# Kernel tuning notes

Measured on AMD Instinct MI355X. Metric: run time of the kernel, lower is better.

The kernel has to match this reference:

```python
import jax, jax.numpy as jnp
import numpy as np

C = 112       # channels, divisible by NCHUNK
NCHUNK = 7    # shift_sizes[0]
PAD = 3       # shift_sizes[0] // 2
EPS = 1e-5


def _gn(x, g, b):
    # GroupNorm(1, C): normalize over (C, D, H, W) per sample, per-channel affine
    mu = jnp.mean(x, axis=(1, 2, 3, 4), keepdims=True)
    var = jnp.mean((x - mu) ** 2, axis=(1, 2, 3, 4), keepdims=True)
    xn = (x - mu) * jax.lax.rsqrt(var + EPS)
    return xn * g[None, :, None, None, None] + b[None, :, None, None, None]


def _conv1x1(x, w, b):
    # 1x1x1 Conv3d == channel-mixing GEMM
    return jnp.einsum('oc,bcdhw->bodhw', w, x) + b[None, :, None, None, None]


def _gelu(x):
    return jax.nn.gelu(x, approximate=False)  # torch nn.GELU default = exact erf


def _pad3(x):
    return jnp.pad(x, ((0, 0), (0, 0), (PAD, PAD), (PAD, PAD), (PAD, PAD)))


def _axial_shift(xp, axis, D, H, W):
    # chunk channels into NCHUNK groups, roll group i by (i - PAD) along `axis`,
    # concat, then narrow each spatial axis at offset PAD with ORIGINAL lengths
    chunks = jnp.split(xp, NCHUNK, axis=1)
    shifted = [jnp.roll(c, s, axis=axis) for c, s in zip(chunks, range(-PAD, PAD + 1))]
    xc = jnp.concatenate(shifted, axis=1)
    return xc[:, :, PAD:PAD + D, PAD:PAD + H, PAD:PAD + W]


def setup_inputs() -> dict:
    key = jax.random.key(0)
    ks = jax.random.split(key, 9)
    B, D, H, W = 1, 64, 64, 64
    hid = 4 * C

    def w(k, shape, fan_in):
        return jax.random.normal(k, shape, jnp.float32) * np.float32(1.0 / np.sqrt(fan_in))

    return {
        'x': jax.random.normal(ks[0], (B, C, D, H, W), jnp.float32),
        'conv1_w': w(ks[1], (C, C), C), 'conv1_b': jnp.zeros((C,), jnp.float32),
        'conv2d_w': w(ks[2], (C, C), C), 'conv2d_b': jnp.zeros((C,), jnp.float32),
        'conv2h_w': w(ks[3], (C, C), C), 'conv2h_b': jnp.zeros((C,), jnp.float32),
        'conv2w_w': w(ks[4], (C, C), C), 'conv2w_b': jnp.zeros((C,), jnp.float32),
        'conv3_w': w(ks[5], (C, C), C), 'conv3_b': jnp.zeros((C,), jnp.float32),
        'fc1_w': w(ks[6], (hid, C), C), 'fc1_b': jnp.zeros((hid,), jnp.float32),
        'fc2_w': w(ks[7], (C, hid), hid), 'fc2_b': jnp.zeros((C,), jnp.float32),
        'n1_g': jnp.ones((C,), jnp.float32), 'n1_b': jnp.zeros((C,), jnp.float32),
        'na1_g': jnp.ones((C,), jnp.float32), 'na1_b': jnp.zeros((C,), jnp.float32),
        'na2_g': jnp.ones((C,), jnp.float32), 'na2_b': jnp.zeros((C,), jnp.float32),
        'n2_g': jnp.ones((C,), jnp.float32), 'n2_b': jnp.zeros((C,), jnp.float32),
    }


def reference(x, conv1_w, conv1_b, conv2d_w, conv2d_b, conv2h_w, conv2h_b,
              conv2w_w, conv2w_b, conv3_w, conv3_b, fc1_w, fc1_b, fc2_w, fc2_b,
              n1_g, n1_b, na1_g, na1_b, na2_g, na2_b, n2_g, n2_b):
    B, _, D, H, W = x.shape
    shortcut = x
    h0 = _gn(x, n1_g, n1_b)                                   # block norm1

    # ---- AxialShift.axial_shift_single_scale ----
    a = _gelu(_gn(_conv1x1(h0, conv1_w, conv1_b), na1_g, na1_b))
    xp = _pad3(a)                                             # padded once (D branch)
    x_d = _gelu(_conv1x1(_axial_shift(xp, 2, D, H, W), conv2d_w, conv2d_b))
    xp = _pad3(xp)                                            # padded twice (H branch, as in source)
    x_h = _gelu(_conv1x1(_axial_shift(xp, 3, D, H, W), conv2h_w, conv2h_b))
    xp = _pad3(xp)                                            # padded thrice (W branch)
    x_w = _gelu(_conv1x1(_axial_shift(xp, 4, D, H, W), conv2w_w, conv2w_b))
    y = _conv1x1(_gn(x_d + x_h + x_w, na2_g, na2_b), conv3_w, conv3_b)
    y = y + h0                                                # AxialShift residual (x_masked == 0)

    x1 = shortcut + y                                         # block residual 1
    m = _gn(x1, n2_g, n2_b)                                   # block norm2
    m = _conv1x1(_gelu(_conv1x1(m, fc1_w, fc1_b)), fc2_w, fc2_b)  # Mlp (drop=0)
    return x1 + m
```

## Files before the change

### kernel.cpp

```cpp
#include <hip/hip_runtime.h>
#include <math.h>

static constexpr int CH   = 112;
static constexpr int HID  = 448;
static constexpr int NPOS = 64 * 64 * 64;
static constexpr long long NELEM = (long long)CH * NPOS;

typedef _Float16 f16x8 __attribute__((ext_vector_type(8)));
typedef _Float16 f16x4 __attribute__((ext_vector_type(4)));
typedef float    f32x4 __attribute__((ext_vector_type(4)));

__device__ __forceinline__ float gelu_f(float x) {
    float ax = fabsf(x) * 0.70710678118654752f;
    float t  = __builtin_amdgcn_rcpf(1.0f + 0.3275911f * ax);
    float p  = t * (0.254829592f + t * (-0.284496736f + t * (1.421413741f +
               t * (-1.453152027f + t * 1.061405429f))));
    float e  = exp2f(-1.4426950408889634f * ax * ax);
    float er = 1.0f - p * e;
    er = (x < 0.f) ? -er : er;
    return 0.5f * x * (1.0f + er);
}

__device__ __forceinline__ void stats_from(const double* __restrict__ S, float* mu, float* inv) {
    double m = S[0] / (double)NELEM;
    double v = S[1] / (double)NELEM - m * m;
    *mu  = (float)m;
    *inv = (float)(1.0 / sqrt(v + 1e-5));
}

__device__ __forceinline__ void block_reduce2(double s, double q, double* __restrict__ out) {
    #pragma unroll
    for (int off = 32; off > 0; off >>= 1) {
        s += __shfl_down(s, off, 64);
        q += __shfl_down(q, off, 64);
    }
    __shared__ double red[16];
    int lane = threadIdx.x & 63, wv = threadIdx.x >> 6;
    int nw = blockDim.x >> 6;
    if (lane == 0) { red[wv] = s; red[wv + 8] = q; }
    __syncthreads();
    if (threadIdx.x == 0) {
        double S = 0, Q = 0;
        for (int i = 0; i < nw; i++) { S += red[i]; Q += red[i + 8]; }
        atomicAdd(out, S);
        atomicAdd(out + 1, Q);
    }
}

__device__ __forceinline__ void mfma_tile(const _Float16* __restrict__ w,
                                          const _Float16 (*lsT)[136],
                                          int l15, int l4, int wv, f32x4 acc[7]) {
    #pragma unroll
    for (int kk = 0; kk < 4; kk++) {
        f16x8 b = *(const f16x8*)(&lsT[wv * 16 + l15][kk * 32 + l4 * 8]);
        #pragma unroll
        for (int mt = 0; mt < 7; mt++) {
            f16x8 a = *(const f16x8*)(w + (mt * 16 + l15) * 128 + kk * 32 + l4 * 8);
            acc[mt] = __builtin_amdgcn_mfma_f32_16x16x32_f16(a, b, acc[mt], 0, 0, 0);
        }
    }
}

__device__ __forceinline__ void accum_gelu(f32x4 tot[7], const f32x4 acc[7],
                                           const float* __restrict__ b, int l4) {
    #pragma unroll
    for (int mt = 0; mt < 7; mt++) {
        float4 bb = *(const float4*)(b + mt * 16 + l4 * 4);
        tot[mt][0] += gelu_f(acc[mt][0] + bb.x);
        tot[mt][1] += gelu_f(acc[mt][1] + bb.y);
        tot[mt][2] += gelu_f(acc[mt][2] + bb.z);
        tot[mt][3] += gelu_f(acc[mt][3] + bb.w);
    }
}

__global__ void k_reduce(const float* __restrict__ x, double* __restrict__ S) {
    long long i0 = (long long)blockIdx.x * blockDim.x + threadIdx.x;
    long long stride = (long long)gridDim.x * blockDim.x;
    const float4* x4 = (const float4*)x;
    long long n4 = NELEM / 4;
    double s = 0, q = 0;
    for (long long i = i0; i < n4; i += stride) {
        float4 v = x4[i];
        s += (double)v.x + (double)v.y + (double)v.z + (double)v.w;
        q += (double)v.x * v.x + (double)v.y * v.y + (double)v.z * v.z + (double)v.w * v.w;
    }
    block_reduce2(s, q, S);
}

__global__ void k_fold(const double* __restrict__ S, const float* __restrict__ w,
                       const float* __restrict__ b, const float* __restrict__ g,
                       const float* __restrict__ bta,
                       _Float16* __restrict__ w16, float* __restrict__ beff) {
    int o = blockIdx.x;
    float mu, inv; stats_from(S, &mu, &inv);
    float partial = 0.f;
    for (int c = threadIdx.x; c < 128; c += blockDim.x) {
        float wv_ = 0.f, contrib = 0.f;
        if (c < CH) {
            float sc = inv * g[c];
            float sh = bta[c] - mu * sc;
            float w0 = w[o * CH + c];
            wv_ = w0 * sc;
            contrib = w0 * sh;
        }
        w16[o * 128 + c] = (_Float16)wv_;
        partial += contrib;
    }
    #pragma unroll
    for (int off = 32; off > 0; off >>= 1) partial += __shfl_down(partial, off, 64);
    __shared__ float rp[2];
    int lane = threadIdx.x & 63, wv_ = threadIdx.x >> 6;
    if (lane == 0) rp[wv_] = partial;
    __syncthreads();
    if (threadIdx.x == 0) beff[o] = b[o] + rp[0] + rp[1];
}

__global__ void k_cast(const float* __restrict__ w2d, const float* __restrict__ w2h,
                       const float* __restrict__ w2w, const float* __restrict__ fc2w,
                       _Float16* __restrict__ w2dh, _Float16* __restrict__ w2hh,
                       _Float16* __restrict__ w2wh, _Float16* __restrict__ fc2h) {
    int b = blockIdx.x;
    if (b < CH) {
        for (int c = threadIdx.x; c < 128; c += blockDim.x) {
            float vd = 0.f, vh = 0.f, vw = 0.f;
            if (c < CH) { vd = w2d[b * CH + c]; vh = w2h[b * CH + c]; vw = w2w[b * CH + c]; }
            w2dh[b * 128 + c] = (_Float16)vd;
            w2hh[b * 128 + c] = (_Float16)vh;
            w2wh[b * 128 + c] = (_Float16)vw;
        }
    }
    for (int i = threadIdx.x; i < CH; i += blockDim.x)
        fc2h[b * CH + i] = (_Float16)fc2w[b * CH + i];
}

__global__ void __launch_bounds__(256, 2)
k_conv1(const float* __restrict__ x, const _Float16* __restrict__ w1h,
        const float* __restrict__ b1e, _Float16* __restrict__ t16, double* __restrict__ S1) {
    __shared__ __align__(16) _Float16 lxT[64][136];
    int tid = threadIdx.x, lane = tid & 63, wv = tid >> 6, l15 = lane & 15, l4 = lane >> 4;
    int pos0 = blockIdx.x * 64;

    {
        int c0 = tid >> 4, q = tid & 15;
        #pragma unroll
        for (int p = 0; p < 7; p++) {
            int c = p * 16 + c0;
            float4 v = *(const float4*)(x + (long long)c * NPOS + pos0 + q * 4);
            lxT[q * 4 + 0][c] = (_Float16)v.x;
            lxT[q * 4 + 1][c] = (_Float16)v.y;
            lxT[q * 4 + 2][c] = (_Float16)v.z;
            lxT[q * 4 + 3][c] = (_Float16)v.w;
        }
        for (int i = tid; i < 64 * 16; i += 256) lxT[i >> 4][112 + (i & 15)] = (_Float16)0.f;
    }
    __syncthreads();

    f32x4 acc[7];
    {
        f32x4 z = {0.f, 0.f, 0.f, 0.f};
        #pragma unroll
        for (int mt = 0; mt < 7; mt++) acc[mt] = z;
    }
    mfma_tile(w1h, lxT, l15, l4, wv, acc);

    long long posw = pos0 + wv * 16 + l15;
    double s = 0, q = 0;
    #pragma unroll
    for (int mt = 0; mt < 7; mt++) {
        int ob = mt * 16 + l4 * 4;
        float4 bb = *(const float4*)(b1e + ob);
        const float* bp = (const float*)&bb;
        f16x4 o4;
        #pragma unroll
        for (int r = 0; r < 4; r++) {
            float tv = acc[mt][r] + bp[r];
            o4[r] = (_Float16)tv;
            s += (double)tv; q += (double)tv * tv;
        }
        *(f16x4*)(t16 + posw * 128 + ob) = o4;
    }
    {
        f16x4 z4; z4[0] = z4[1] = z4[2] = z4[3] = (_Float16)0.f;
        *(f16x4*)(t16 + posw * 128 + 112 + l4 * 4) = z4;
    }
    block_reduce2(s, q, S1);
}

__global__ void k_act(const _Float16* __restrict__ t16, _Float16* __restrict__ a16,
                      const double* __restrict__ S1, const float* __restrict__ g,
                      const float* __restrict__ bta) {
    float mu, inv; stats_from(S1, &mu, &inv);
    long long i8 = (long long)blockIdx.x * blockDim.x + threadIdx.x;
    int c = (int)((i8 * 8) & 127);
    f16x8 r;
    if (c < 112) {
        f16x8 v = *(const f16x8*)(t16 + i8 * 8);
        float4 g0 = *(const float4*)(g + c);
        float4 g1 = *(const float4*)(g + c + 4);
        float4 b0 = *(const float4*)(bta + c);
        float4 b1 = *(const float4*)(bta + c + 4);
        const float* gp0 = (const float*)&g0; const float* gp1 = (const float*)&g1;
        const float* bp0 = (const float*)&b0; const float* bp1 = (const float*)&b1;
        #pragma unroll
        for (int j = 0; j < 4; j++) {
            float sc = inv * gp0[j], sh = bp0[j] - mu * sc;
            r[j] = (_Float16)gelu_f((float)v[j] * sc + sh);
        }
        #pragma unroll
        for (int j = 0; j < 4; j++) {
            float sc = inv * gp1[j], sh = bp1[j] - mu * sc;
            r[4 + j] = (_Float16)gelu_f((float)v[4 + j] * sc + sh);
        }
    } else {
        #pragma unroll
        for (int j = 0; j < 8; j++) r[j] = (_Float16)0.f;
    }
    *(f16x8*)(a16 + i8 * 8) = r;
}

__global__ void __launch_bounds__(256, 2)
k_shift(const _Float16* __restrict__ a16,
        const _Float16* __restrict__ w2dh, const float* __restrict__ b2d,
        const _Float16* __restrict__ w2hh, const float* __restrict__ b2h,
        const _Float16* __restrict__ w2wh, const float* __restrict__ b2w,
        _Float16* __restrict__ s16, double* __restrict__ S2) {
    __shared__ __align__(16) _Float16 lsT[64][136];
    int tid = threadIdx.x, lane = tid & 63, wv = tid >> 6, l15 = lane & 15, l4 = lane >> 4;
    int d = blockIdx.x >> 6, h = blockIdx.x & 63;

    f32x4 tot[7], acc[7];
    {
        f32x4 z = {0.f, 0.f, 0.f, 0.f};
        #pragma unroll
        for (int mt = 0; mt < 7; mt++) tot[mt] = z;
    }
    f16x8 z8;
    #pragma unroll
    for (int j = 0; j < 8; j++) z8[j] = (_Float16)0.f;

    for (int u = tid; u < 1024; u += 256) {
        int w = u >> 4, u16 = u & 15;
        f16x8 v = z8;
        if (u16 < 14) {
            int p = u16 >> 1;
            int dd = d - (p - 3);
            if ((unsigned)dd < 64u)
                v = *(const f16x8*)(a16 + (long long)(dd * 4096 + h * 64 + w) * 128 + u16 * 8);
        }
        *(f16x8*)(&lsT[w][u16 * 8]) = v;
    }
    __syncthreads();
    {
        f32x4 z = {0.f, 0.f, 0.f, 0.f};
        #pragma unroll
        for (int mt = 0; mt < 7; mt++) acc[mt] = z;
    }
    mfma_tile(w2dh, lsT, l15, l4, wv, acc);
    accum_gelu(tot, acc, b2d, l4);
    __syncthreads();

    {
        int dd = d - 3;
        bool dok = (unsigned)dd < 64u;
        for (int u = tid; u < 1024; u += 256) {
            int w = u >> 4, u16 = u & 15;
            f16x8 v = z8;
            if (u16 < 14) {
                int p = u16 >> 1;
                int hh = h - p;
                int ww = w - 3;
                if (dok && (unsigned)hh < 64u && ww >= 0)
                    v = *(const f16x8*)(a16 + (long long)(dd * 4096 + hh * 64 + ww) * 128 + u16 * 8);
            }
            *(f16x8*)(&lsT[w][u16 * 8]) = v;
        }
    }
    __syncthreads();
    {
        f32x4 z = {0.f, 0.f, 0.f, 0.f};
        #pragma unroll
        for (int mt = 0; mt < 7; mt++) acc[mt] = z;
    }
    mfma_tile(w2hh, lsT, l15, l4, wv, acc);
    accum_gelu(tot, acc, b2h, l4);
    __syncthreads();

    {
        int dd = d - 6, hh = h - 6;
        bool ok = ((unsigned)dd < 64u) && ((unsigned)hh < 64u);
        for (int u = tid; u < 1024; u += 256) {
            int w = u >> 4, u16 = u & 15;
            f16x8 v = z8;
            if (ok && u16 < 14) {
                int p = u16 >> 1;
                int ww = w - 3 - p;
                if ((unsigned)ww < 64u)
                    v = *(const f16x8*)(a16 + (long long)(dd * 4096 + hh * 64 + ww) * 128 + u16 * 8);
            }
            *(f16x8*)(&lsT[w][u16 * 8]) = v;
        }
    }
    __syncthreads();
    {
        f32x4 z = {0.f, 0.f, 0.f, 0.f};
        #pragma unroll
        for (int mt = 0; mt < 7; mt++) acc[mt] = z;
    }
    mfma_tile(w2wh, lsT, l15, l4, wv, acc);
    accum_gelu(tot, acc, b2w, l4);

    long long posw = d * 4096 + h * 64 + wv * 16 + l15;
    double s = 0, q = 0;
    #pragma unroll
    for (int mt = 0; mt < 7; mt++) {
        f16x4 o4;
        #pragma unroll
        for (int r = 0; r < 4; r++) {
            float sv = tot[mt][r];
            o4[r] = (_Float16)sv;
            s += (double)sv; q += (double)sv * sv;
        }
        *(f16x4*)(s16 + posw * 128 + mt * 16 + l4 * 4) = o4;
    }
    {
        f16x4 z4; z4[0] = z4[1] = z4[2] = z4[3] = (_Float16)0.f;
        *(f16x4*)(s16 + posw * 128 + 112 + l4 * 4) = z4;
    }
    block_reduce2(s, q, S2);
}

__global__ void __launch_bounds__(256, 2)
k_comb(const _Float16* s16, const float* __restrict__ x,
       const _Float16* __restrict__ w3h, const float* __restrict__ b3e,
       const double* __restrict__ S0, const float* __restrict__ n1g,
       const float* __restrict__ n1b, float* __restrict__ x1,
       _Float16* x1h, double* __restrict__ S3) {
    __shared__ __align__(16) _Float16 lsT[64][136];
    int tid = threadIdx.x, lane = tid & 63, wv = tid >> 6, l15 = lane & 15, l4 = lane >> 4;
    int pos0 = blockIdx.x * 64;

    for (int u = tid; u < 1024; u += 256) {
        int w = u >> 4, u16 = u & 15;
        *(f16x8*)(&lsT[w][u16 * 8]) =
            *(const f16x8*)(s16 + (long long)(pos0 + w) * 128 + u16 * 8);
    }
    __syncthreads();

    f32x4 acc[7];
    {
        f32x4 z = {0.f, 0.f, 0.f, 0.f};
        #pragma unroll
        for (int mt = 0; mt < 7; mt++) acc[mt] = z;
    }
    mfma_tile(w3h, lsT, l15, l4, wv, acc);

    float mu, inv; stats_from(S0, &mu, &inv);
    long long posw = pos0 + wv * 16 + l15;
    double s = 0, q = 0;
    #pragma unroll
    for (int mt = 0; mt < 7; mt++) {
        int ob = mt * 16 + l4 * 4;
        float4 b3 = *(const float4*)(b3e + ob);
        float4 g4 = *(const float4*)(n1g + ob);
        float4 n4 = *(const float4*)(n1b + ob);
        const float* b3p = (const float*)&b3;
        const float* g4p = (const float*)&g4;
        const float* n4p = (const float*)&n4;
        f16x4 o4;
        #pragma unroll
        for (int r = 0; r < 4; r++) {
            int o = ob + r;
            float y  = acc[mt][r] + b3p[r];
            float xv = x[(long long)o * NPOS + posw];
            float sc = inv * g4p[r];
            float h0 = xv * sc + (n4p[r] - mu * sc);
            float v  = xv + y + h0;
            x1[(long long)o * NPOS + posw] = v;
            o4[r] = (_Float16)v;
            s += (double)v; q += (double)v * v;
        }
        *(f16x4*)(x1h + posw * 128 + ob) = o4;
    }
    block_reduce2(s, q, S3);
}

__global__ void __launch_bounds__(256, 3)
k_mlp(float* __restrict__ x1out, const _Float16* __restrict__ x1h,
      const _Float16* __restrict__ fc1h, const float* __restrict__ b1m,
      const _Float16* __restrict__ fc2h, const float* __restrict__ fc2b) {
    __shared__ __align__(16) char smem[64 * 232 * 2];
    _Float16 (*lxT)[136] = (_Float16 (*)[136])smem;
    _Float16 (*GT)[232]  = (_Float16 (*)[232])smem;
    int tid = threadIdx.x, lane = tid & 63, wv = tid >> 6, l15 = lane & 15, l4 = lane >> 4;
    int pos0 = blockIdx.x * 64;

    for (int u = tid; u < 1024; u += 256) {
        int w = u >> 4, u16 = u & 15;
        *(f16x8*)(&lxT[w][u16 * 8]) =
            *(const f16x8*)(x1h + (long long)(pos0 + w) * 128 + u16 * 8);
    }
    __syncthreads();

    int hb = wv * 112;
    f32x4 acc1[7][4];
    {
        f32x4 z = {0.f, 0.f, 0.f, 0.f};
        #pragma unroll
        for (int mt = 0; mt < 7; mt++)
            #pragma unroll
            for (int nt = 0; nt < 4; nt++) acc1[mt][nt] = z;
    }
    #pragma unroll
    for (int kk = 0; kk < 4; kk++) {
        f16x8 a[7];
        #pragma unroll
        for (int mt = 0; mt < 7; mt++)
            a[mt] = *(const f16x8*)(fc1h + (hb + mt * 16 + l15) * 128 + kk * 32 + l4 * 8);
        #pragma unroll
        for (int nt = 0; nt < 4; nt++) {
            f16x8 b = *(const f16x8*)(&lxT[nt * 16 + l15][kk * 32 + l4 * 8]);
            #pragma unroll
            for (int mt = 0; mt < 7; mt++)
                acc1[mt][nt] = __builtin_amdgcn_mfma_f32_16x16x32_f16(a[mt], b, acc1[mt][nt], 0, 0, 0);
        }
    }
    f16x4 g16[7][4];
    #pragma unroll
    for (int mt = 0; mt < 7; mt++) {
        float4 bias = *(const float4*)(b1m + hb + mt * 16 + l4 * 4);
        #pragma unroll
        for (int nt = 0; nt < 4; nt++) {
            g16[mt][nt][0] = (_Float16)gelu_f(acc1[mt][nt][0] + bias.x);
            g16[mt][nt][1] = (_Float16)gelu_f(acc1[mt][nt][1] + bias.y);
            g16[mt][nt][2] = (_Float16)gelu_f(acc1[mt][nt][2] + bias.z);
            g16[mt][nt][3] = (_Float16)gelu_f(acc1[mt][nt][3] + bias.w);
        }
    }
    __syncthreads();

    int pw = wv * 16 + l15;
    f32x4 acc2[7];
    {
        f32x4 z = {0.f, 0.f, 0.f, 0.f};
        #pragma unroll
        for (int mt = 0; mt < 7; mt++) acc2[mt] = z;
    }
    #pragma unroll
    for (int ph = 0; ph < 2; ph++) {
        if ((wv >> 1) == ph) {
            int cb = (wv & 1) * 112;
            #pragma unroll
            for (int mt = 0; mt < 7; mt++) {
                int col = cb + mt * 16 + l4 * 4;
                #pragma unroll
                for (int nt = 0; nt < 4; nt++)
                    *(f16x4*)(&GT[nt * 16 + l15][col]) = g16[mt][nt];
            }
        }
        __syncthreads();
        #pragma unroll
        for (int kk = 0; kk < 7; kk++) {
            f16x8 b = *(const f16x8*)(&GT[pw][kk * 32 + l4 * 8]);
            #pragma unroll
            for (int mt = 0; mt < 7; mt++) {
                f16x8 a = *(const f16x8*)(fc2h + (mt * 16 + l15) * 448 + ph * 224 + kk * 32 + l4 * 8);
                acc2[mt] = __builtin_amdgcn_mfma_f32_16x16x32_f16(a, b, acc2[mt], 0, 0, 0);
            }
        }
        if (ph == 0) __syncthreads();
    }

    long long gp = pos0 + pw;
    #pragma unroll
    for (int mt = 0; mt < 7; mt++) {
        int ob = mt * 16 + l4 * 4;
        float4 b2 = *(const float4*)(fc2b + ob);
        float bb[4] = {b2.x, b2.y, b2.z, b2.w};
        #pragma unroll
        for (int r = 0; r < 4; r++) {
            long long idx = (long long)(ob + r) * NPOS + gp;
            x1out[idx] = x1out[idx] + acc2[mt][r] + bb[r];
        }
    }
}

extern "C" void kernel_launch(void* const* d_in, const int* in_sizes, int n_in,
                              void* d_out, int out_size, void* d_ws, size_t ws_size,
                              hipStream_t stream) {
    const float* x       = (const float*)d_in[0];
    const float* conv1_w = (const float*)d_in[1];
    const float* conv1_b = (const float*)d_in[2];
    const float* conv2d_w= (const float*)d_in[3];
    const float* conv2d_b= (const float*)d_in[4];
    const float* conv2h_w= (const float*)d_in[5];
    const float* conv2h_b= (const float*)d_in[6];
    const float* conv2w_w= (const float*)d_in[7];
    const float* conv2w_b= (const float*)d_in[8];
    const float* conv3_w = (const float*)d_in[9];
    const float* conv3_b = (const float*)d_in[10];
    const float* fc1_w   = (const float*)d_in[11];
    const float* fc1_b   = (const float*)d_in[12];
    const float* fc2_w   = (const float*)d_in[13];
    const float* fc2_b   = (const float*)d_in[14];
    const float* n1_g    = (const float*)d_in[15];
    const float* n1_b    = (const float*)d_in[16];
    const float* na1_g   = (const float*)d_in[17];
    const float* na1_b   = (const float*)d_in[18];
    const float* na2_g   = (const float*)d_in[19];
    const float* na2_b   = (const float*)d_in[20];
    const float* n2_g    = (const float*)d_in[21];
    const float* n2_b    = (const float*)d_in[22];

    char* ws = (char*)d_ws;
    double* S = (double*)ws;
    float* b1e = (float*)(ws + 512);
    float* b3e = b1e + 112;
    float* b1m = b3e + 112;
    _Float16* w1h  = (_Float16*)(ws + 3200);
    _Float16* w3h  = w1h  + 112 * 128;
    _Float16* w2dh = w3h  + 112 * 128;
    _Float16* w2hh = w2dh + 112 * 128;
    _Float16* w2wh = w2hh + 112 * 128;
    _Float16* fc1h = w2wh + 112 * 128;
    _Float16* fc2h = fc1h + 448 * 128;
    float* bufA = (float*)(ws + (1 << 20));
    _Float16* t16 = (_Float16*)bufA;
    _Float16* s16 = (_Float16*)bufA;
    _Float16* x1h = (_Float16*)bufA;
    float* out  = (float*)d_out;
    _Float16* a16 = (_Float16*)out;

    hipMemsetAsync(S, 0, 8 * sizeof(double), stream);
    k_cast<<<448, 128, 0, stream>>>(conv2d_w, conv2h_w, conv2w_w, fc2_w,
                                    w2dh, w2hh, w2wh, fc2h);
    k_reduce<<<1024, 256, 0, stream>>>(x, S);
    k_fold<<<112, 128, 0, stream>>>(S, conv1_w, conv1_b, n1_g, n1_b, w1h, b1e);
    k_conv1<<<4096, 256, 0, stream>>>(x, w1h, b1e, t16, S + 2);
    k_act<<<16384, 256, 0, stream>>>(t16, a16, S + 2, na1_g, na1_b);
    k_shift<<<4096, 256, 0, stream>>>(a16, w2dh, conv2d_b, w2hh, conv2h_b,
                                      w2wh, conv2w_b, s16, S + 4);
    k_fold<<<112, 128, 0, stream>>>(S + 4, conv3_w, conv3_b, na2_g, na2_b, w3h, b3e);
    k_comb<<<4096, 256, 0, stream>>>(s16, x, w3h, b3e, S, n1_g, n1_b, out, x1h, S + 6);
    k_fold<<<448, 128, 0, stream>>>(S + 6, fc1_w, fc1_b, n2_g, n2_b, fc1h, b1m);
    k_mlp<<<4096, 256, 0, stream>>>(out, x1h, fc1h, b1m, fc2h, fc2_b);
}
```

Baseline: 1.126 ms.

## Stage fc2 weights in LDS with double-buffered seven-phase pipeline in MLP kernel

Reassigns fc1 hidden rows so each wave's output tiles are interleaved across 64-wide hidden chunks. This lets the fc2 GEMM be split into seven K-phases of 64. Each phase double-buffers both the GELU activations and a 112x64 slice of fc2 weights in shared memory, so weights come from LDS instead of per-wave global loads. The cost is more barriers, larger LDS use per block (lower occupancy possible), and cooperative weight copies in every block.

Result: slower. 2.018 ms (+79.2%).

```diff
diff --git a/kernel.cpp b/kernel.cpp
--- a/kernel.cpp
+++ b/kernel.cpp
@@ -388,9 +388,10 @@
 k_mlp(float* __restrict__ x1out, const _Float16* __restrict__ x1h,
       const _Float16* __restrict__ fc1h, const float* __restrict__ b1m,
       const _Float16* __restrict__ fc2h, const float* __restrict__ fc2b) {
-    __shared__ __align__(16) char smem[64 * 232 * 2];
-    _Float16 (*lxT)[136] = (_Float16 (*)[136])smem;
-    _Float16 (*GT)[232]  = (_Float16 (*)[232])smem;
+    __shared__ __align__(16) char smem[2 * 64 * 72 * 2 + 2 * 112 * 72 * 2];
+    _Float16 (*lxT)[136]    = (_Float16 (*)[136])smem;
+    _Float16 (*GT)[64][72]  = (_Float16 (*)[64][72])smem;
+    _Float16 (*wA)[112][72] = (_Float16 (*)[112][72])(smem + 2 * 64 * 72 * 2);
     int tid = threadIdx.x, lane = tid & 63, wv = tid >> 6, l15 = lane & 15, l4 = lane >> 4;
     int pos0 = blockIdx.x * 64;
 
@@ -401,7 +402,6 @@
     }
     __syncthreads();
 
-    int hb = wv * 112;
     f32x4 acc1[7][4];
     {
         f32x4 z = {0.f, 0.f, 0.f, 0.f};
@@ -415,7 +415,7 @@
         f16x8 a[7];
         #pragma unroll
         for (int mt = 0; mt < 7; mt++)
-            a[mt] = *(const f16x8*)(fc1h + (hb + mt * 16 + l15) * 128 + kk * 32 + l4 * 8);
+            a[mt] = *(const f16x8*)(fc1h + (mt * 64 + wv * 16 + l15) * 128 + kk * 32 + l4 * 8);
         #pragma unroll
         for (int nt = 0; nt < 4; nt++) {
             f16x8 b = *(const f16x8*)(&lxT[nt * 16 + l15][kk * 32 + l4 * 8]);
@@ -427,7 +427,7 @@
     f16x4 g16[7][4];
     #pragma unroll
     for (int mt = 0; mt < 7; mt++) {
-        float4 bias = *(const float4*)(b1m + hb + mt * 16 + l4 * 4);
+        float4 bias = *(const float4*)(b1m + mt * 64 + wv * 16 + l4 * 4);
         #pragma unroll
         for (int nt = 0; nt < 4; nt++) {
             g16[mt][nt][0] = (_Float16)gelu_f(acc1[mt][nt][0] + bias.x);
@@ -445,29 +445,40 @@
         #pragma unroll
         for (int mt = 0; mt < 7; mt++) acc2[mt] = z;
     }
-    #pragma unroll
-    for (int ph = 0; ph < 2; ph++) {
-        if ((wv >> 1) == ph) {
-            int cb = (wv & 1) * 112;
+
+    #pragma unroll
+    for (int nt = 0; nt < 4; nt++)
+        *(f16x4*)(&GT[0][nt * 16 + l15][wv * 16 + l4 * 4]) = g16[0][nt];
+    for (int u = tid; u < 896; u += 256) {
+        int o = u >> 3, kg = u & 7;
+        *(f16x8*)(&wA[0][o][kg * 8]) = *(const f16x8*)(fc2h + o * 448 + kg * 8);
+    }
+    __syncthreads();
+
+    #pragma unroll
+    for (int p = 0; p < 7; p++) {
+        const int buf = p & 1;
+        if (p < 6) {
+            const int nb = buf ^ 1;
+            #pragma unroll
+            for (int nt = 0; nt < 4; nt++)
+                *(f16x4*)(&GT[nb][nt * 16 + l15][wv * 16 + l4 * 4]) = g16[p + 1][nt];
+            for (int u = tid; u < 896; u += 256) {
+                int o = u >> 3, kg = u & 7;
+                *(f16x8*)(&wA[nb][o][kg * 8]) =
+                    *(const f16x8*)(fc2h + o * 448 + (p + 1) * 64 + kg * 8);
+            }
+        }
+        #pragma unroll
+        for (int kk = 0; kk < 2; kk++) {
+            f16x8 b = *(const f16x8*)(&GT[buf][pw][kk * 32 + l4 * 8]);
             #pragma unroll
             for (int mt = 0; mt < 7; mt++) {
-                int col = cb + mt * 16 + l4 * 4;
-                #pragma unroll
-                for (int nt = 0; nt < 4; nt++)
-                    *(f16x4*)(&GT[nt * 16 + l15][col]) = g16[mt][nt];
-            }
-        }
-        __syncthreads();
-        #pragma unroll
-        for (int kk = 0; kk < 7; kk++) {
-            f16x8 b = *(const f16x8*)(&GT[pw][kk * 32 + l4 * 8]);
-            #pragma unroll
-            for (int mt = 0; mt < 7; mt++) {
-                f16x8 a = *(const f16x8*)(fc2h + (mt * 16 + l15) * 448 + ph * 224 + kk * 32 + l4 * 8);
+                f16x8 a = *(const f16x8*)(&wA[buf][mt * 16 + l15][kk * 32 + l4 * 8]);
                 acc2[mt] = __builtin_amdgcn_mfma_f32_16x16x32_f16(a, b, acc2[mt], 0, 0, 0);
             }
         }
-        if (ph == 0) __syncthreads();
+        __syncthreads();
     }
 
     long long gp = pos0 + pw;
```

## Make MLP waves independent per 16-position tile, removing block-wide syncs

Applied to the files above, without the earlier changes.

Restructures k_mlp so each wave owns 16 positions and computes all 448 hidden units for them in two halves, keeping the x1 tile in registers instead of staging it through shared memory. The GELU output goes to a per-wave shared-memory slice that only that wave reads, so every __syncthreads is removed. The aim is to drop block-wide barriers and the LDS staging of the input. In exchange each wave now loads the full fc1 and fc2 weight sets from global or cache, which adds weight traffic, and relies on lgkmcnt waits for intra-wave LDS ordering.

After: 1.213 ms. 1.08x slower.

```diff
diff --git a/kernel.cpp b/kernel.cpp
--- a/kernel.cpp
+++ b/kernel.cpp
@@ -388,86 +388,65 @@
 k_mlp(float* __restrict__ x1out, const _Float16* __restrict__ x1h,
       const _Float16* __restrict__ fc1h, const float* __restrict__ b1m,
       const _Float16* __restrict__ fc2h, const float* __restrict__ fc2b) {
-    __shared__ __align__(16) char smem[64 * 232 * 2];
-    _Float16 (*lxT)[136] = (_Float16 (*)[136])smem;
-    _Float16 (*GT)[232]  = (_Float16 (*)[232])smem;
+    __shared__ __align__(16) _Float16 GTq[4][16][232];
     int tid = threadIdx.x, lane = tid & 63, wv = tid >> 6, l15 = lane & 15, l4 = lane >> 4;
     int pos0 = blockIdx.x * 64;
-
-    for (int u = tid; u < 1024; u += 256) {
-        int w = u >> 4, u16 = u & 15;
-        *(f16x8*)(&lxT[w][u16 * 8]) =
-            *(const f16x8*)(x1h + (long long)(pos0 + w) * 128 + u16 * 8);
-    }
-    __syncthreads();
-
-    int hb = wv * 112;
-    f32x4 acc1[7][4];
-    {
-        f32x4 z = {0.f, 0.f, 0.f, 0.f};
-        #pragma unroll
-        for (int mt = 0; mt < 7; mt++)
+    int pw = wv * 16 + l15;
+
+    f16x8 bx[4];
+    {
+        long long rowb = (long long)(pos0 + pw) * 128;
+        #pragma unroll
+        for (int kk = 0; kk < 4; kk++)
+            bx[kk] = *(const f16x8*)(x1h + rowb + kk * 32 + l4 * 8);
+    }
+
+    f32x4 acc2[7];
+    {
+        f32x4 z = {0.f, 0.f, 0.f, 0.f};
+        #pragma unroll
+        for (int mt = 0; mt < 7; mt++) acc2[mt] = z;
+    }
+
+    #pragma unroll
+    for (int hf = 0; hf < 2; hf++) {
+        f32x4 acc1[14];
+        {
+            f32x4 z = {0.f, 0.f, 0.f, 0.f};
             #pragma unroll
-            for (int nt = 0; nt < 4; nt++) acc1[mt][nt] = z;
-    }
-    #pragma unroll
-    for (int kk = 0; kk < 4; kk++) {
-        f16x8 a[7];
-        #pragma unroll
-        for (int mt = 0; mt < 7; mt++)
-            a[mt] = *(const f16x8*)(fc1h + (hb + mt * 16 + l15) * 128 + kk * 32 + l4 * 8);
-        #pragma unroll
-        for (int nt = 0; nt < 4; nt++) {
-            f16x8 b = *(const f16x8*)(&lxT[nt * 16 + l15][kk * 32 + l4 * 8]);
+            for (int mt = 0; mt < 14; mt++) acc1[mt] = z;
+        }
+        #pragma unroll
+        for (int kk = 0; kk < 4; kk++) {
             #pragma unroll
-            for (int mt = 0; mt < 7; mt++)
-                acc1[mt][nt] = __builtin_amdgcn_mfma_f32_16x16x32_f16(a[mt], b, acc1[mt][nt], 0, 0, 0);
-        }
-    }
-    f16x4 g16[7][4];
-    #pragma unroll
-    for (int mt = 0; mt < 7; mt++) {
-        float4 bias = *(const float4*)(b1m + hb + mt * 16 + l4 * 4);
-        #pragma unroll
-        for (int nt = 0; nt < 4; nt++) {
-            g16[mt][nt][0] = (_Float16)gelu_f(acc1[mt][nt][0] + bias.x);
-            g16[mt][nt][1] = (_Float16)gelu_f(acc1[mt][nt][1] + bias.y);
-            g16[mt][nt][2] = (_Float16)gelu_f(acc1[mt][nt][2] + bias.z);
-            g16[mt][nt][3] = (_Float16)gelu_f(acc1[mt][nt][3] + bias.w);
-        }
-    }
-    __syncthreads();
-
-    int pw = wv * 16 + l15;
-    f32x4 acc2[7];
-    {
-        f32x4 z = {0.f, 0.f, 0.f, 0.f};
-        #pragma unroll
-        for (int mt = 0; mt < 7; mt++) acc2[mt] = z;
-    }
-    #pragma unroll
-    for (int ph = 0; ph < 2; ph++) {
-        if ((wv >> 1) == ph) {
-            int cb = (wv & 1) * 112;
+            for (int mt = 0; mt < 14; mt++) {
+                f16x8 a = *(const f16x8*)(fc1h + (hf * 224 + mt * 16 + l15) * 128 + kk * 32 + l4 * 8);
+                acc1[mt] = __builtin_amdgcn_mfma_f32_16x16x32_f16(a, bx[kk], acc1[mt], 0, 0, 0);
+            }
+        }
+        asm volatile("s_waitcnt lgkmcnt(0)" ::: "memory");
+        __builtin_amdgcn_sched_barrier(0);
+        #pragma unroll
+        for (int mt = 0; mt < 14; mt++) {
+            float4 bias = *(const float4*)(b1m + hf * 224 + mt * 16 + l4 * 4);
+            f16x4 g4;
+            g4[0] = (_Float16)gelu_f(acc1[mt][0] + bias.x);
+            g4[1] = (_Float16)gelu_f(acc1[mt][1] + bias.y);
+            g4[2] = (_Float16)gelu_f(acc1[mt][2] + bias.z);
+            g4[3] = (_Float16)gelu_f(acc1[mt][3] + bias.w);
+            *(f16x4*)(&GTq[wv][l15][mt * 16 + l4 * 4]) = g4;
+        }
+        asm volatile("s_waitcnt lgkmcnt(0)" ::: "memory");
+        __builtin_amdgcn_sched_barrier(0);
+        #pragma unroll
+        for (int kk2 = 0; kk2 < 7; kk2++) {
+            f16x8 b = *(const f16x8*)(&GTq[wv][l15][kk2 * 32 + l4 * 8]);
             #pragma unroll
             for (int mt = 0; mt < 7; mt++) {
-                int col = cb + mt * 16 + l4 * 4;
-                #pragma unroll
-                for (int nt = 0; nt < 4; nt++)
-                    *(f16x4*)(&GT[nt * 16 + l15][col]) = g16[mt][nt];
-            }
-        }
-        __syncthreads();
-        #pragma unroll
-        for (int kk = 0; kk < 7; kk++) {
-            f16x8 b = *(const f16x8*)(&GT[pw][kk * 32 + l4 * 8]);
-            #pragma unroll
-            for (int mt = 0; mt < 7; mt++) {
-                f16x8 a = *(const f16x8*)(fc2h + (mt * 16 + l15) * 448 + ph * 224 + kk * 32 + l4 * 8);
+                f16x8 a = *(const f16x8*)(fc2h + (mt * 16 + l15) * 448 + hf * 224 + kk2 * 32 + l4 * 8);
                 acc2[mt] = __builtin_amdgcn_mfma_f32_16x16x32_f16(a, b, acc2[mt], 0, 0, 0);
             }
         }
-        if (ph == 0) __syncthreads();
     }
 
     long long gp = pos0 + pw;
```
